# Optimization experiments

Measured on AMD Instinct MI355X. Metric: run time of the kernel, lower is better.

Reference implementation:

```python
import jax, jax.numpy as jnp
import numpy as np

T, N, E = 24, 50000, 800000
IN_F, HID, OUT_F, K = 11, 128, 3, 2


def setup_inputs() -> dict:
    key = jax.random.key(0)
    ks = jax.random.split(key, 8)
    X_seq = jax.random.normal(ks[0], (T, N, IN_F), jnp.float32)
    # monotone time channel (col 6) so dt = X[t+1][:,6] - X[t][:,6] > 0 in the rollout
    times = 0.1 * jnp.arange(T, dtype=jnp.float32)
    X_seq = X_seq.at[:, :, 6].set(jnp.broadcast_to(times[:, None], (T, N)))
    edge_index = jax.random.randint(ks[1], (2, E), 0, N, dtype=jnp.int32)
    s = 0.1
    Wx = s * jax.random.normal(ks[2], (3, K, IN_F, HID), jnp.float32)
    bx = s * jax.random.normal(ks[3], (3, HID), jnp.float32)
    Wh = s * jax.random.normal(ks[4], (3, K, HID, HID), jnp.float32)
    bh = s * jax.random.normal(ks[5], (3, HID), jnp.float32)
    W_head = s * jax.random.normal(ks[6], (HID, OUT_F), jnp.float32)
    b_head = s * jax.random.normal(ks[7], (OUT_F,), jnp.float32)
    return {"X_seq": X_seq, "edge_index": edge_index, "Wx": Wx, "bx": bx,
            "Wh": Wh, "bh": bh, "W_head": W_head, "b_head": b_head}


def reference(X_seq, edge_index, Wx, bx, Wh, bh, W_head, b_head):
    n = X_seq.shape[1]
    src, dst = edge_index[0], edge_index[1]
    # PyG ChebConv sym-normalized scaled Laplacian with lambda_max=2:
    # L_hat = -D^{-1/2} A D^{-1/2}  (zero diagonal)
    deg = jax.ops.segment_sum(jnp.ones(src.shape[0], X_seq.dtype), src, num_segments=n)
    dinv = jnp.where(deg > 0, 1.0 / jnp.sqrt(deg), 0.0)
    w = -(dinv[src] * dinv[dst])  # [E]

    def lap(x):  # x: [N, F] -> L_hat @ x via gather/scatter over edges
        return jax.ops.segment_sum(w[:, None] * x[src], dst, num_segments=n)

    def cheb(x, W, b):  # K=2 ChebConv: Tx0 @ W0 + (L_hat x) @ W1 + bias
        return x @ W[0] + lap(x) @ W[1] + b

    def gru(x, h):  # GConvGRU cell
        z = jax.nn.sigmoid(cheb(x, Wx[0], bx[0]) + cheb(h, Wh[0], bh[0]))
        r = jax.nn.sigmoid(cheb(x, Wx[1], bx[1]) + cheb(h, Wh[1], bh[1]))
        h_tilde = jnp.tanh(cheb(x, Wx[2], bx[2]) + cheb(h * r, Wh[2], bh[2]))
        return z * h + (1.0 - z) * h_tilde

    hid = W_head.shape[0]
    h0 = gru(X_seq[0], jnp.zeros((n, hid), X_seq.dtype))
    u0 = h0 @ W_head + b_head  # [N, 3]
    dt = X_seq[1:, :, 6] - X_seq[:-1, :, 6]  # [T-1, N]

    def step(carry, inp):
        h, u_prev, prev_pos = carry
        x_orig, dt_t = inp
        pos = jax.lax.stop_gradient(u_prev)        # next_u = u.detach()
        vel = (pos - prev_pos) / dt_t[:, None]     # X[t+1][:,8:11]
        x = jnp.concatenate([x_orig[:, :3], pos, x_orig[:, 6:8], vel], axis=1)
        h = gru(x, h)
        u = h @ W_head + b_head
        return (h, u, pos), u

    _, outs = jax.lax.scan(step, (h0, u0, X_seq[0, :, 3:6]), (X_seq[1:], dt))
    return jnp.concatenate([u0[None], outs], axis=0)  # [T, N, 3]
```

## Files before the change

### kernel.cpp

```cpp
#include <hip/hip_runtime.h>
#include <math.h>

#define NN 50000
#define EE 800000
#define TT 24
#define INF 11
#define HID 128

static constexpr int KTOT = 280;
#define BM 64
#define BN 128
#define BK 8

__device__ __forceinline__ float fast_sigmoid(float v) {
    float e = __expf(-v);
    return __builtin_amdgcn_rcpf(1.0f + e);
}
__device__ __forceinline__ float fast_tanh(float v) {
    float e2 = __expf(2.0f * v);
    return 1.0f - 2.0f * __builtin_amdgcn_rcpf(e2 + 1.0f);
}


__global__ void count_deg_kernel(const int* __restrict__ src, const int* __restrict__ dst,
                                 int* __restrict__ deg_src, int* __restrict__ cnt_dst) {
    int e = blockIdx.x * blockDim.x + threadIdx.x;
    if (e < EE) {
        atomicAdd(&deg_src[src[e]], 1);
        atomicAdd(&cnt_dst[dst[e]], 1);
    }
}

__global__ void dinv_kernel(const int* __restrict__ deg, float* __restrict__ dinv) {
    int i = blockIdx.x * blockDim.x + threadIdx.x;
    if (i < NN) {
        int d = deg[i];
        dinv[i] = (d > 0) ? 1.0f / sqrtf((float)d) : 0.0f;
    }
}

__global__ void scan_kernel(const int* __restrict__ cnt, int* __restrict__ row_ptr) {
    __shared__ int buf[2][1024];
    __shared__ int carry_s;
    int tid = threadIdx.x;
    if (tid == 0) carry_s = 0;
    __syncthreads();
    for (int base = 0; base < NN; base += 1024) {
        int i = base + tid;
        int v = (i < NN) ? cnt[i] : 0;
        int pb = 0;
        buf[0][tid] = v;
        __syncthreads();
        for (int off = 1; off < 1024; off <<= 1) {
            int t = buf[pb][tid] + ((tid >= off) ? buf[pb][tid - off] : 0);
            buf[pb ^ 1][tid] = t;
            pb ^= 1;
            __syncthreads();
        }
        int incl = buf[pb][tid];
        int carry = carry_s;
        if (i < NN) row_ptr[i] = carry + incl - v;
        __syncthreads();
        if (tid == 0) carry_s = carry + buf[pb][1023];
        __syncthreads();
    }
    if (tid == 0) row_ptr[NN] = carry_s;
}

__global__ void fill_csr_kernel(const int* __restrict__ src, const int* __restrict__ dst,
                                const int* __restrict__ row_ptr, int* __restrict__ fillp,
                                const float* __restrict__ dinv,
                                int2* __restrict__ csr) {
    int e = blockIdx.x * blockDim.x + threadIdx.x;
    if (e < EE) {
        int s = src[e], d = dst[e];
        int p = row_ptr[d] + atomicAdd(&fillp[d], 1);
        float w = -(dinv[s] * dinv[d]);
        csr[p] = make_int2(s, __float_as_int(w));
    }
}

__global__ void pack_weights_kernel(const float* __restrict__ Wx, const float* __restrict__ bx,
                                    const float* __restrict__ Wh, const float* __restrict__ bh,
                                    float* __restrict__ WA, float* __restrict__ biasA,
                                    float* __restrict__ WB, float* __restrict__ biasB) {
    int idx = blockIdx.x * blockDim.x + threadIdx.x;
    const int NA = 280 * 256, NB = 280 * 128;
    if (idx < NA) {
        int k = idx / 256, j = idx % 256;
        int g = j >> 7, jj = j & 127;
        float v = 0.0f;
        if (k < 12)       { if (k < 11)      v = Wx[((g*2 + 0)*11 + k)      * 128 + jj]; }
        else if (k < 24)  { int kk = k - 12; if (kk < 11) v = Wx[((g*2 + 1)*11 + kk) * 128 + jj]; }
        else if (k < 152) { int kk = k - 24;  v = Wh[((g*2 + 0)*128 + kk) * 128 + jj]; }
        else              { int kk = k - 152; v = Wh[((g*2 + 1)*128 + kk) * 128 + jj]; }
        WA[idx] = v;
    } else if (idx < NA + NB) {
        int t = idx - NA;
        int k = t / 128, jj = t % 128;
        float v = 0.0f;
        if (k < 12)       { if (k < 11)      v = Wx[(4*11 + k)  * 128 + jj]; }
        else if (k < 24)  { int kk = k - 12; if (kk < 11) v = Wx[(5*11 + kk) * 128 + jj]; }
        else if (k < 152) { int kk = k - 24;  v = Wh[(4*128 + kk) * 128 + jj]; }
        else              { int kk = k - 152; v = Wh[(5*128 + kk) * 128 + jj]; }
        WB[t] = v;
    } else if (idx < NA + NB + 256) {
        int j = idx - (NA + NB);
        int g = j >> 7, jj = j & 127;
        biasA[j] = bx[g*128 + jj] + bh[g*128 + jj];
    } else if (idx < NA + NB + 256 + 128) {
        int jj = idx - (NA + NB + 256);
        biasB[jj] = bx[2*128 + jj] + bh[2*128 + jj];
    }
}


__global__ void copy_x0_kernel(const float* __restrict__ X0, float* __restrict__ x) {
    int i = blockIdx.x * blockDim.x + threadIdx.x;
    if (i < NN) {
        #pragma unroll
        for (int c = 0; c < 11; c++) x[i*12 + c] = X0[i*11 + c];
        x[i*12 + 11] = 0.0f;
    }
}

__global__ void build_x_kernel(const float* __restrict__ Xt, const float* __restrict__ Xtm1,
                               const float* __restrict__ pos, const float* __restrict__ prevbase,
                               int prev_stride, int prev_off, float* __restrict__ x) {
    int i = blockIdx.x * blockDim.x + threadIdx.x;
    if (i >= NN) return;
    const float* xo = Xt + (size_t)i * 11;
    float tnow  = xo[6];
    float tprev = Xtm1[(size_t)i * 11 + 6];
    float inv = 1.0f / (tnow - tprev);
    float p0 = pos[(size_t)i*3 + 0], p1 = pos[(size_t)i*3 + 1], p2 = pos[(size_t)i*3 + 2];
    const float* pp = prevbase + (size_t)i * prev_stride + prev_off;
    float q0 = pp[0], q1 = pp[1], q2 = pp[2];
    float* xr = x + (size_t)i * 12;
    xr[0] = xo[0]; xr[1] = xo[1]; xr[2] = xo[2];
    xr[3] = p0;    xr[4] = p1;    xr[5] = p2;
    xr[6] = tnow;  xr[7] = xo[7];
    xr[8] = (p0 - q0) * inv; xr[9] = (p1 - q1) * inv; xr[10] = (p2 - q2) * inv;
    xr[11] = 0.0f;
}

__global__ void lap_small_kernel(const int* __restrict__ row_ptr, const int2* __restrict__ csr,
                                 const float* __restrict__ x, float* __restrict__ xl) {
    int node = blockIdx.x * 16 + (threadIdx.x >> 4);
    int f = threadIdx.x & 15;
    if (node >= NN) return;
    int b = row_ptr[node], e = row_ptr[node + 1];
    float acc = 0.0f;
    for (int p = b; p < e; p++) {
        int2 ed = csr[p];
        float w = __int_as_float(ed.y);
        if (f < 12) acc += w * x[(size_t)ed.x*12 + f];
    }
    if (f < 12) xl[(size_t)node*12 + f] = acc;
}

__global__ void lap_big_kernel(const int* __restrict__ row_ptr, const int2* __restrict__ csr,
                               const float* __restrict__ hin, float* __restrict__ hout) {
    int node = blockIdx.x * 8 + threadIdx.y;
    if (node >= NN) return;
    int f = threadIdx.x;
    const float4* h4 = (const float4*)hin;
    float4 acc0 = make_float4(0.f, 0.f, 0.f, 0.f);
    float4 acc1 = make_float4(0.f, 0.f, 0.f, 0.f);
    int b = row_ptr[node], e = row_ptr[node + 1];
    int p = b;
    for (; p + 1 < e; p += 2) {
        int2 e0 = csr[p];
        int2 e1 = csr[p + 1];
        float w0 = __int_as_float(e0.y);
        float w1 = __int_as_float(e1.y);
        float4 v0 = h4[(size_t)e0.x*32 + f];
        float4 v1 = h4[(size_t)e1.x*32 + f];
        acc0.x += w0 * v0.x; acc0.y += w0 * v0.y; acc0.z += w0 * v0.z; acc0.w += w0 * v0.w;
        acc1.x += w1 * v1.x; acc1.y += w1 * v1.y; acc1.z += w1 * v1.z; acc1.w += w1 * v1.w;
    }
    if (p < e) {
        int2 e0 = csr[p];
        float w0 = __int_as_float(e0.y);
        float4 v0 = h4[(size_t)e0.x*32 + f];
        acc0.x += w0 * v0.x; acc0.y += w0 * v0.y; acc0.z += w0 * v0.z; acc0.w += w0 * v0.w;
    }
    acc0.x += acc1.x; acc0.y += acc1.y; acc0.z += acc1.z; acc0.w += acc1.w;
    ((float4*)hout)[(size_t)node*32 + f] = acc0;
}

__device__ __forceinline__ float2 loadA2(const float* __restrict__ x, const float* __restrict__ xl,
                                         const float* __restrict__ a2, const float* __restrict__ a3,
                                         int row, int k) {
    if (k < 12)  return *(const float2*)(x  + (size_t)row*12  + k);
    if (k < 24)  return *(const float2*)(xl + (size_t)row*12  + (k - 12));
    if (k < 152) return *(const float2*)(a2 + (size_t)row*128 + (k - 24));
    return *(const float2*)(a3 + (size_t)row*128 + (k - 152));
}

template<int NOUT, int EPI>
__global__ __launch_bounds__(256)
void gemm_kernel(const float* __restrict__ x, const float* __restrict__ xl,
                 const float* __restrict__ a2, const float* __restrict__ a3,
                 const float* __restrict__ W, const float* __restrict__ bias,
                 float* __restrict__ p0, float* __restrict__ p1,
                 const float* __restrict__ p2)
{
    __shared__ float As[BK][BM];
    __shared__ float Bs[BK][BN];
    const int tid = threadIdx.x;
    const int row0 = blockIdx.x * BM;
    const int col0 = blockIdx.y * BN;
    const int tn_g = tid & 31;
    const int tm_g = tid >> 5;
    const int lm = tid >> 2;
    const int kp = (tid & 3) * 2;
    int arow = row0 + lm; if (arow >= NN) arow = NN - 1;
    const int kb = tid >> 5;
    const int cb = (tid & 31) * 4;

    float acc[8][4];
    #pragma unroll
    for (int i = 0; i < 8; i++) { acc[i][0]=0.f; acc[i][1]=0.f; acc[i][2]=0.f; acc[i][3]=0.f; }

    for (int k0 = 0; k0 < KTOT; k0 += BK) {
        float2 av = loadA2(x, xl, a2, a3, arow, k0 + kp);
        float4 bv = *(const float4*)(W + (size_t)(k0 + kb) * NOUT + col0 + cb);
        __syncthreads();
        As[kp][lm]     = av.x;
        As[kp + 1][lm] = av.y;
        *(float4*)(&Bs[kb][cb]) = bv;
        __syncthreads();
        #pragma unroll
        for (int kk = 0; kk < BK; kk++) {
            float4 a0 = *(const float4*)(&As[kk][tm_g*8]);
            float4 a1 = *(const float4*)(&As[kk][tm_g*8 + 4]);
            float4 b  = *(const float4*)(&Bs[kk][tn_g*4]);
            float av_[8] = {a0.x, a0.y, a0.z, a0.w, a1.x, a1.y, a1.z, a1.w};
            float bv_[4] = {b.x, b.y, b.z, b.w};
            #pragma unroll
            for (int i = 0; i < 8; i++)
                #pragma unroll
                for (int j = 0; j < 4; j++)
                    acc[i][j] += av_[i] * bv_[j];
        }
    }

    #pragma unroll
    for (int i = 0; i < 8; i++) {
        int row = row0 + tm_g*8 + i;
        if (row >= NN) continue;
        #pragma unroll
        for (int j = 0; j < 4; j++) {
            int col = col0 + tn_g*4 + j;
            float v = acc[i][j] + bias[col];
            if (EPI == 0) {
                float s = fast_sigmoid(v);
                if (col < HID) {
                    p0[(size_t)row*HID + col] = s;
                } else {
                    int c = col - HID;
                    p1[(size_t)row*HID + c] = p2[(size_t)row*HID + c] * s;
                }
            } else {
                float ht = fast_tanh(v);
                float zz   = p0[(size_t)row*HID + col];
                float hold = p1[(size_t)row*HID + col];
                p1[(size_t)row*HID + col] = zz*hold + (1.0f - zz)*ht;
            }
        }
    }
}

__global__ void head_kernel(const float* __restrict__ h, const float* __restrict__ Whead,
                            const float* __restrict__ bhead, float* __restrict__ out) {
    int node = blockIdx.x * 4 + (threadIdx.x >> 6);
    int lane = threadIdx.x & 63;
    if (node >= NN) return;
    float h0 = h[(size_t)node*128 + lane];
    float h1 = h[(size_t)node*128 + 64 + lane];
    float p[3];
    #pragma unroll
    for (int j = 0; j < 3; j++)
        p[j] = h0 * Whead[lane*3 + j] + h1 * Whead[(64 + lane)*3 + j];
    #pragma unroll
    for (int off = 32; off > 0; off >>= 1) {
        p[0] += __shfl_down(p[0], off);
        p[1] += __shfl_down(p[1], off);
        p[2] += __shfl_down(p[2], off);
    }
    if (lane == 0) {
        out[(size_t)node*3 + 0] = p[0] + bhead[0];
        out[(size_t)node*3 + 1] = p[1] + bhead[1];
        out[(size_t)node*3 + 2] = p[2] + bhead[2];
    }
}


extern "C" void kernel_launch(void* const* d_in, const int* in_sizes, int n_in,
                              void* d_out, int out_size, void* d_ws, size_t ws_size,
                              hipStream_t stream) {
    const float* X_seq  = (const float*)d_in[0];
    const int*   eidx   = (const int*)  d_in[1];
    const float* Wx     = (const float*)d_in[2];
    const float* bx     = (const float*)d_in[3];
    const float* Wh     = (const float*)d_in[4];
    const float* bh     = (const float*)d_in[5];
    const float* Whead  = (const float*)d_in[6];
    const float* bhead  = (const float*)d_in[7];
    float* out = (float*)d_out;

    const int* src = eidx;
    const int* dst = eidx + EE;

    char* base = (char*)d_ws;
    size_t off = 0;
    auto carve = [&](size_t bytes) -> void* {
        void* p = base + off;
        off += (bytes + 255) & ~(size_t)255;
        return p;
    };
    int*   deg_i   = (int*)  carve((size_t)NN * 4);
    int*   cnt     = (int*)  carve((size_t)NN * 4);
    int*   fillp   = (int*)  carve((size_t)NN * 4);
    int*   row_ptr = (int*)  carve((size_t)(NN + 1) * 4);
    float* dinv    = (float*)carve((size_t)NN * 4);
    int2*  csr     = (int2*) carve((size_t)EE * 8);
    float* WA      = (float*)carve((size_t)280 * 256 * 4);
    float* biasA   = (float*)carve(256 * 4);
    float* WB      = (float*)carve((size_t)280 * 128 * 4);
    float* biasB   = (float*)carve(128 * 4);
    float* xbuf    = (float*)carve((size_t)NN * 12 * 4);
    float* xlbuf   = (float*)carve((size_t)NN * 12 * 4);
    float* hbuf    = (float*)carve((size_t)NN * 128 * 4);
    float* hlbuf   = (float*)carve((size_t)NN * 128 * 4);
    float* hrbuf   = (float*)carve((size_t)NN * 128 * 4);
    float* zbuf    = (float*)carve((size_t)NN * 128 * 4);
    float* hrlbuf  = hlbuf;
    (void)ws_size; (void)n_in; (void)in_sizes; (void)out_size;

    hipMemsetAsync(deg_i, 0, (size_t)NN * 4, stream);
    hipMemsetAsync(cnt,   0, (size_t)NN * 4, stream);
    hipMemsetAsync(fillp, 0, (size_t)NN * 4, stream);
    hipMemsetAsync(hbuf,  0, (size_t)NN * 128 * 4, stream);

    count_deg_kernel<<<(EE + 255) / 256, 256, 0, stream>>>(src, dst, deg_i, cnt);
    dinv_kernel<<<(NN + 255) / 256, 256, 0, stream>>>(deg_i, dinv);
    scan_kernel<<<1, 1024, 0, stream>>>(cnt, row_ptr);
    fill_csr_kernel<<<(EE + 255) / 256, 256, 0, stream>>>(src, dst, row_ptr, fillp, dinv, csr);
    {
        int total = 280*256 + 280*128 + 256 + 128;
        pack_weights_kernel<<<(total + 255) / 256, 256, 0, stream>>>(Wx, bx, Wh, bh, WA, biasA, WB, biasB);
    }

    const int gridN256 = (NN + 255) / 256;
    const dim3 gridGA((NN + BM - 1) / BM, 2);
    const dim3 gridGB((NN + BM - 1) / BM, 1);

    for (int t = 0; t < TT; t++) {
        if (t == 0) {
            copy_x0_kernel<<<gridN256, 256, 0, stream>>>(X_seq, xbuf);
        } else {
            const float* Xt   = X_seq + (size_t)t * NN * 11;
            const float* Xtm1 = X_seq + (size_t)(t - 1) * NN * 11;
            const float* pos  = out + (size_t)(t - 1) * NN * 3;
            const float* prevbase;
            int pstride, poff;
            if (t == 1) { prevbase = X_seq; pstride = 11; poff = 3; }
            else        { prevbase = out + (size_t)(t - 2) * NN * 3; pstride = 3; poff = 0; }
            build_x_kernel<<<gridN256, 256, 0, stream>>>(Xt, Xtm1, pos, prevbase, pstride, poff, xbuf);
        }

        lap_small_kernel<<<(NN + 15) / 16, 256, 0, stream>>>(row_ptr, csr, xbuf, xlbuf);
        lap_big_kernel<<<(NN + 7) / 8, dim3(32, 8), 0, stream>>>(row_ptr, csr, hbuf, hlbuf);

        gemm_kernel<256, 0><<<gridGA, 256, 0, stream>>>(xbuf, xlbuf, hbuf, hlbuf, WA, biasA,
                                                        zbuf, hrbuf, hbuf);
        lap_big_kernel<<<(NN + 7) / 8, dim3(32, 8), 0, stream>>>(row_ptr, csr, hrbuf, hrlbuf);

        gemm_kernel<128, 1><<<gridGB, 256, 0, stream>>>(xbuf, xlbuf, hrbuf, hrlbuf, WB, biasB,
                                                        zbuf, hbuf, nullptr);

        head_kernel<<<(NN + 3) / 4, 256, 0, stream>>>(hbuf, Whead, bhead, out + (size_t)t * NN * 3);
    }
}
```

Measured before the change: 8.278 ms.

## Double-buffer GEMM shared tiles and split Laplacian edges across half-waves

The GEMM kernel now double-buffers its A and B shared-memory tiles. The next K-slice is prefetched into registers while the current slice is computed, which removes one barrier per step and hides global load latency. The big Laplacian kernel now assigns a full 64-lane wavefront to each node. The two 32-lane halves process alternating edges and are combined with a cross-half shuffle, raising memory-level parallelism for the gather. In exchange it uses twice the shared memory in the GEMM and runs twice as many threads per node in the gather.

New measurement: 8.145 ms. Within noise of the previous version (-1.6%).

```diff
diff --git a/kernel.cpp b/kernel.cpp
--- a/kernel.cpp
+++ b/kernel.cpp
@@ -11,6 +11,7 @@
 #define BM 64
 #define BN 128
 #define BK 8
+static constexpr int NSTEP = KTOT / BK;
 
 __device__ __forceinline__ float fast_sigmoid(float v) {
     float e = __expf(-v);
@@ -159,34 +160,48 @@
     if (f < 12) xl[(size_t)node*12 + f] = acc;
 }
 
-__global__ void lap_big_kernel(const int* __restrict__ row_ptr, const int2* __restrict__ csr,
-                               const float* __restrict__ hin, float* __restrict__ hout) {
-    int node = blockIdx.x * 8 + threadIdx.y;
+__global__ __launch_bounds__(256)
+void lap_big_kernel(const int* __restrict__ row_ptr, const int2* __restrict__ csr,
+                    const float* __restrict__ hin, float* __restrict__ hout) {
+    int tid  = threadIdx.x;
+    int node = blockIdx.x * 4 + (tid >> 6);
     if (node >= NN) return;
-    int f = threadIdx.x;
+    int eo = (tid >> 5) & 1;
+    int f  = tid & 31;
     const float4* h4 = (const float4*)hin;
     float4 acc0 = make_float4(0.f, 0.f, 0.f, 0.f);
     float4 acc1 = make_float4(0.f, 0.f, 0.f, 0.f);
     int b = row_ptr[node], e = row_ptr[node + 1];
     int p = b;
+    for (; p + 3 < e; p += 4) {
+        int2 ea = csr[p + eo];
+        int2 eb = csr[p + 2 + eo];
+        float wa = __int_as_float(ea.y);
+        float wb = __int_as_float(eb.y);
+        float4 va = h4[(size_t)ea.x*32 + f];
+        float4 vb = h4[(size_t)eb.x*32 + f];
+        acc0.x += wa * va.x; acc0.y += wa * va.y; acc0.z += wa * va.z; acc0.w += wa * va.w;
+        acc1.x += wb * vb.x; acc1.y += wb * vb.y; acc1.z += wb * vb.z; acc1.w += wb * vb.w;
+    }
     for (; p + 1 < e; p += 2) {
-        int2 e0 = csr[p];
-        int2 e1 = csr[p + 1];
-        float w0 = __int_as_float(e0.y);
-        float w1 = __int_as_float(e1.y);
-        float4 v0 = h4[(size_t)e0.x*32 + f];
-        float4 v1 = h4[(size_t)e1.x*32 + f];
-        acc0.x += w0 * v0.x; acc0.y += w0 * v0.y; acc0.z += w0 * v0.z; acc0.w += w0 * v0.w;
-        acc1.x += w1 * v1.x; acc1.y += w1 * v1.y; acc1.z += w1 * v1.z; acc1.w += w1 * v1.w;
-    }
-    if (p < e) {
-        int2 e0 = csr[p];
-        float w0 = __int_as_float(e0.y);
-        float4 v0 = h4[(size_t)e0.x*32 + f];
-        acc0.x += w0 * v0.x; acc0.y += w0 * v0.y; acc0.z += w0 * v0.z; acc0.w += w0 * v0.w;
+        int2 ea = csr[p + eo];
+        float wa = __int_as_float(ea.y);
+        float4 va = h4[(size_t)ea.x*32 + f];
+        acc0.x += wa * va.x; acc0.y += wa * va.y; acc0.z += wa * va.z; acc0.w += wa * va.w;
+    }
+    if (p < e && eo == 0) {
+        int2 ea = csr[p];
+        float wa = __int_as_float(ea.y);
+        float4 va = h4[(size_t)ea.x*32 + f];
+        acc0.x += wa * va.x; acc0.y += wa * va.y; acc0.z += wa * va.z; acc0.w += wa * va.w;
     }
     acc0.x += acc1.x; acc0.y += acc1.y; acc0.z += acc1.z; acc0.w += acc1.w;
-    ((float4*)hout)[(size_t)node*32 + f] = acc0;
+    acc0.x += __shfl_xor(acc0.x, 32);
+    acc0.y += __shfl_xor(acc0.y, 32);
+    acc0.z += __shfl_xor(acc0.z, 32);
+    acc0.w += __shfl_xor(acc0.w, 32);
+    if (eo == 0)
+        ((float4*)hout)[(size_t)node*32 + f] = acc0;
 }
 
 __device__ __forceinline__ float2 loadA2(const float* __restrict__ x, const float* __restrict__ xl,
@@ -206,8 +221,8 @@
                  float* __restrict__ p0, float* __restrict__ p1,
                  const float* __restrict__ p2)
 {
-    __shared__ float As[BK][BM];
-    __shared__ float Bs[BK][BN];
+    __shared__ float As[2][BK][BM];
+    __shared__ float Bs[2][BK][BN];
     const int tid = threadIdx.x;
     const int row0 = blockIdx.x * BM;
     const int col0 = blockIdx.y * BN;
@@ -223,19 +238,26 @@
     #pragma unroll
     for (int i = 0; i < 8; i++) { acc[i][0]=0.f; acc[i][1]=0.f; acc[i][2]=0.f; acc[i][3]=0.f; }
 
-    for (int k0 = 0; k0 < KTOT; k0 += BK) {
-        float2 av = loadA2(x, xl, a2, a3, arow, k0 + kp);
-        float4 bv = *(const float4*)(W + (size_t)(k0 + kb) * NOUT + col0 + cb);
-        __syncthreads();
-        As[kp][lm]     = av.x;
-        As[kp + 1][lm] = av.y;
-        *(float4*)(&Bs[kb][cb]) = bv;
-        __syncthreads();
+    float2 av = loadA2(x, xl, a2, a3, arow, kp);
+    float4 bv = *(const float4*)(W + (size_t)kb * NOUT + col0 + cb);
+    As[0][kp][lm]     = av.x;
+    As[0][kp + 1][lm] = av.y;
+    *(float4*)(&Bs[0][kb][cb]) = bv;
+    __syncthreads();
+
+    int bb = 0;
+    for (int s = 0; s < NSTEP; s++) {
+        float2 av2; float4 bv2;
+        if (s + 1 < NSTEP) {
+            int kn = (s + 1) * BK;
+            av2 = loadA2(x, xl, a2, a3, arow, kn + kp);
+            bv2 = *(const float4*)(W + (size_t)(kn + kb) * NOUT + col0 + cb);
+        }
         #pragma unroll
         for (int kk = 0; kk < BK; kk++) {
-            float4 a0 = *(const float4*)(&As[kk][tm_g*8]);
-            float4 a1 = *(const float4*)(&As[kk][tm_g*8 + 4]);
-            float4 b  = *(const float4*)(&Bs[kk][tn_g*4]);
+            float4 a0 = *(const float4*)(&As[bb][kk][tm_g*8]);
+            float4 a1 = *(const float4*)(&As[bb][kk][tm_g*8 + 4]);
+            float4 b  = *(const float4*)(&Bs[bb][kk][tn_g*4]);
             float av_[8] = {a0.x, a0.y, a0.z, a0.w, a1.x, a1.y, a1.z, a1.w};
             float bv_[4] = {b.x, b.y, b.z, b.w};
             #pragma unroll
@@ -243,6 +265,13 @@
                 #pragma unroll
                 for (int j = 0; j < 4; j++)
                     acc[i][j] += av_[i] * bv_[j];
+        }
+        if (s + 1 < NSTEP) {
+            As[bb ^ 1][kp][lm]     = av2.x;
+            As[bb ^ 1][kp + 1][lm] = av2.y;
+            *(float4*)(&Bs[bb ^ 1][kb][cb]) = bv2;
+            __syncthreads();
+            bb ^= 1;
         }
     }
 
@@ -372,11 +401,11 @@
         }
 
         lap_small_kernel<<<(NN + 15) / 16, 256, 0, stream>>>(row_ptr, csr, xbuf, xlbuf);
-        lap_big_kernel<<<(NN + 7) / 8, dim3(32, 8), 0, stream>>>(row_ptr, csr, hbuf, hlbuf);
+        lap_big_kernel<<<(NN + 3) / 4, 256, 0, stream>>>(row_ptr, csr, hbuf, hlbuf);
 
         gemm_kernel<256, 0><<<gridGA, 256, 0, stream>>>(xbuf, xlbuf, hbuf, hlbuf, WA, biasA,
                                                         zbuf, hrbuf, hbuf);
-        lap_big_kernel<<<(NN + 7) / 8, dim3(32, 8), 0, stream>>>(row_ptr, csr, hrbuf, hrlbuf);
+        lap_big_kernel<<<(NN + 3) / 4, 256, 0, stream>>>(row_ptr, csr, hrbuf, hrlbuf);
 
         gemm_kernel<128, 1><<<gridGB, 256, 0, stream>>>(xbuf, xlbuf, hrbuf, hrlbuf, WB, biasB,
                                                         zbuf, hbuf, nullptr);
```
